# Kernel tuning notes

Hardware: AMD Instinct MI355X
Metric: run time of the kernel (lower is better)

Reference implementation:

```python
import jax, jax.numpy as jnp
import numpy as np

N_NODES = 100000


def _sage_conv(x, src, dst, W_l, b_l, W_r, num_nodes):
    # PyG SAGEConv (aggr='mean'): out = lin_l(mean_j x_j) + lin_r(x)
    msg = x[src]                                                   # [E, d] gather
    s = jax.ops.segment_sum(msg, dst, num_segments=num_nodes)      # [N, d]
    cnt = jax.ops.segment_sum(jnp.ones((src.shape[0], 1), x.dtype), dst,
                              num_segments=num_nodes)              # [N, 1]
    agg = s / jnp.maximum(cnt, 1)                                  # mean, 0 if no neighbors
    return agg @ W_l.T + b_l + x @ W_r.T


def setup_inputs() -> dict:
    key = jax.random.key(0)
    ks = jax.random.split(key, 8)
    d = 64
    E = 1600000
    scale = 1.0 / np.sqrt(d)
    x = jax.random.normal(ks[0], (N_NODES, d), dtype=jnp.float32)
    edge_index = jax.random.randint(ks[1], (2, E), 0, N_NODES, dtype=jnp.int64)
    W1_l = jax.random.normal(ks[2], (d, d), dtype=jnp.float32) * scale
    b1_l = jnp.zeros((d,), dtype=jnp.float32)
    W1_r = jax.random.normal(ks[3], (d, d), dtype=jnp.float32) * scale
    W2_l = jax.random.normal(ks[4], (d, d), dtype=jnp.float32) * scale
    b2_l = jnp.zeros((d,), dtype=jnp.float32)
    W2_r = jax.random.normal(ks[5], (d, d), dtype=jnp.float32) * scale
    return {"x": x, "edge_index": edge_index, "W1_l": W1_l, "b1_l": b1_l,
            "W1_r": W1_r, "W2_l": W2_l, "b2_l": b2_l, "W2_r": W2_r}


def reference(x, edge_index, W1_l, b1_l, W1_r, W2_l, b2_l, W2_r):
    src, dst = edge_index[0], edge_index[1]
    h = jax.nn.relu(_sage_conv(x, src, dst, W1_l, b1_l, W1_r, N_NODES))
    h = jax.nn.relu(_sage_conv(h, src, dst, W2_l, b2_l, W2_r, N_NODES))
    return h
```

## Files before the change

kernel.cpp:

```cpp
#include <hip/hip_runtime.h>
#include <hip/hip_fp16.h>


#define NFEAT 64
#define NPB 128
#define NBUCK 782
#define MAXPB 2560
#define TILE 4096

typedef _Float16 h8 __attribute__((ext_vector_type(8)));
typedef _Float16 h4 __attribute__((ext_vector_type(4)));
typedef float f4 __attribute__((ext_vector_type(4)));
typedef float f2 __attribute__((ext_vector_type(2)));

__device__ inline h8 cvt8f(const float* p) {
  float4 lo = *(const float4*)p;
  float4 hi = *(const float4*)(p + 4);
  h8 f;
  f[0]=(_Float16)lo.x; f[1]=(_Float16)lo.y; f[2]=(_Float16)lo.z; f[3]=(_Float16)lo.w;
  f[4]=(_Float16)hi.x; f[5]=(_Float16)hi.y; f[6]=(_Float16)hi.z; f[7]=(_Float16)hi.w;
  return f;
}

__device__ inline void acc16(float* a, uint4 r) {
  f2 t;
  t = __builtin_amdgcn_cvt_pk_f32_fp8((int)r.x, false); a[0]+=t[0];  a[1]+=t[1];
  t = __builtin_amdgcn_cvt_pk_f32_fp8((int)r.x, true);  a[2]+=t[0];  a[3]+=t[1];
  t = __builtin_amdgcn_cvt_pk_f32_fp8((int)r.y, false); a[4]+=t[0];  a[5]+=t[1];
  t = __builtin_amdgcn_cvt_pk_f32_fp8((int)r.y, true);  a[6]+=t[0];  a[7]+=t[1];
  t = __builtin_amdgcn_cvt_pk_f32_fp8((int)r.z, false); a[8]+=t[0];  a[9]+=t[1];
  t = __builtin_amdgcn_cvt_pk_f32_fp8((int)r.z, true);  a[10]+=t[0]; a[11]+=t[1];
  t = __builtin_amdgcn_cvt_pk_f32_fp8((int)r.w, false); a[12]+=t[0]; a[13]+=t[1];
  t = __builtin_amdgcn_cvt_pk_f32_fp8((int)r.w, true);  a[14]+=t[0]; a[15]+=t[1];
}

__device__ inline void gather_accum(float* a, const int* __restrict__ csr,
                                    const unsigned char* __restrict__ Z,
                                    int start, int deg, int q) {
  int j = 0;
  for (; j + 8 <= deg; j += 8) {
    int idx[8];
#pragma unroll
    for (int k = 0; k < 8; ++k) idx[k] = csr[start + j + k];
    uint4 r[8];
#pragma unroll
    for (int k = 0; k < 8; ++k)
      r[k] = *(const uint4*)(Z + (size_t)idx[k] * NFEAT + q * 16);
#pragma unroll
    for (int k = 0; k < 8; ++k) acc16(a, r[k]);
  }
  for (; j + 4 <= deg; j += 4) {
    int n0 = csr[start + j + 0];
    int n1 = csr[start + j + 1];
    int n2 = csr[start + j + 2];
    int n3 = csr[start + j + 3];
    uint4 r0 = *(const uint4*)(Z + (size_t)n0 * NFEAT + q * 16);
    uint4 r1 = *(const uint4*)(Z + (size_t)n1 * NFEAT + q * 16);
    uint4 r2 = *(const uint4*)(Z + (size_t)n2 * NFEAT + q * 16);
    uint4 r3 = *(const uint4*)(Z + (size_t)n3 * NFEAT + q * 16);
    acc16(a, r0); acc16(a, r1); acc16(a, r2); acc16(a, r3);
  }
  for (; j < deg; ++j) {
    int nb = csr[start + j];
    uint4 r = *(const uint4*)(Z + (size_t)nb * NFEAT + q * 16);
    acc16(a, r);
  }
}

__global__ __launch_bounds__(512) void build_gemm1_k(
    const int* __restrict__ src, const int* __restrict__ dst,
    int* __restrict__ gcur, int* __restrict__ pairs, int E, int sb,
    const float* __restrict__ X, const float* __restrict__ Wl,
    const float* __restrict__ Wr, const float* __restrict__ bias,
    unsigned char* __restrict__ Zf8, __half* __restrict__ Ph, int n) {
  int tid = threadIdx.x;
  if ((int)blockIdx.x < sb) {
    __shared__ int lcnt[NBUCK];
    __shared__ int loff[NBUCK];
    __shared__ int lcur[NBUCK];
    __shared__ int lbase[NBUCK];
    __shared__ int s_packed[TILE];
    __shared__ unsigned short s_b[TILE];

    int tileStart = blockIdx.x * TILE;
    int tileCnt = E - tileStart; if (tileCnt > TILE) tileCnt = TILE;

    for (int t = tid; t < NBUCK; t += 512) lcnt[t] = 0;
    __syncthreads();

    int ep[8], eb[8];
    int base = tileStart + tid * 8;
    int ne = 0;
    if (base + 7 < E) {
      int4 a0 = *(const int4*)(src + base);
      int4 a1 = *(const int4*)(src + base + 4);
      int4 b0 = *(const int4*)(dst + base);
      int4 b1 = *(const int4*)(dst + base + 4);
      int es[8] = {a0.x,a0.y,a0.z,a0.w,a1.x,a1.y,a1.z,a1.w};
      int ed[8] = {b0.x,b0.y,b0.z,b0.w,b1.x,b1.y,b1.z,b1.w};
#pragma unroll
      for (int j = 0; j < 8; ++j) {
        eb[j] = ed[j] >> 7;
        ep[j] = es[j] | ((ed[j] & 127) << 17);
      }
      ne = 8;
    } else {
      for (int j = 0; j < 8 && base + j < E; ++j) {
        int s = src[base + j], d = dst[base + j];
        eb[j] = d >> 7;
        ep[j] = s | ((d & 127) << 17);
        ++ne;
      }
    }
    for (int j = 0; j < ne; ++j) atomicAdd(&lcnt[eb[j]], 1);
    __syncthreads();

    if (tid < 64) {
      int carry = 0;
      for (int cb = 0; cb < NBUCK; cb += 64) {
        int i = cb + tid;
        int v = (i < NBUCK) ? lcnt[i] : 0;
        int x = v;
#pragma unroll
        for (int d = 1; d < 64; d <<= 1) {
          int y = __shfl_up(x, d);
          if (tid >= d) x += y;
        }
        if (i < NBUCK) { int e = x - v + carry; loff[i] = e; lcur[i] = e; }
        carry += __shfl(x, 63);
      }
    }
    __syncthreads();

    for (int t = tid; t < NBUCK; t += 512) {
      int v = lcnt[t];
      if (v) lbase[t] = atomicAdd(&gcur[t], v);
    }
    __syncthreads();

    for (int j = 0; j < ne; ++j) {
      int b = eb[j];
      int slot = atomicAdd(&lcur[b], 1);
      s_packed[slot] = ep[j];
      s_b[slot] = (unsigned short)b;
    }
    __syncthreads();

    for (int k = tid; k < tileCnt; k += 512) {
      int b = s_b[k];
      int g = lbase[b] + (k - loff[b]);
      if (g < MAXPB) pairs[(size_t)b * MAXPB + g] = s_packed[k];
    }
  } else {
    int wave = tid >> 6, lane = tid & 63;
    int m = lane & 15, quad = lane >> 4;
    int row0 = (((int)blockIdx.x - sb) * 8 + wave) * 16;
    if (row0 >= n) return;

    h8 wf[2][4][2];
#pragma unroll
    for (int mat = 0; mat < 2; ++mat) {
      const float* W = mat ? Wr : Wl;
#pragma unroll
      for (int t = 0; t < 4; ++t)
#pragma unroll
        for (int s = 0; s < 2; ++s)
          wf[mat][t][s] = cvt8f(W + (t * 16 + m) * 64 + s * 32 + quad * 8);
    }

    int rowm = row0 + m; if (rowm > n - 1) rowm = n - 1;
    const float* xp = X + (size_t)rowm * 64 + quad * 8;
    h8 af0 = cvt8f(xp);
    h8 af1 = cvt8f(xp + 32);

    f4 accz[4], accp[4];
#pragma unroll
    for (int t = 0; t < 4; ++t) {
      f4 z; z[0]=0.f; z[1]=0.f; z[2]=0.f; z[3]=0.f;
      float4 bl = *(const float4*)(bias + t * 16 + quad * 4);
      f4 p; p[0]=bl.x; p[1]=bl.y; p[2]=bl.z; p[3]=bl.w;
      z = __builtin_amdgcn_mfma_f32_16x16x32_f16(wf[0][t][0], af0, z, 0, 0, 0);
      z = __builtin_amdgcn_mfma_f32_16x16x32_f16(wf[0][t][1], af1, z, 0, 0, 0);
      p = __builtin_amdgcn_mfma_f32_16x16x32_f16(wf[1][t][0], af0, p, 0, 0, 0);
      p = __builtin_amdgcn_mfma_f32_16x16x32_f16(wf[1][t][1], af1, p, 0, 0, 0);
      accz[t] = z;
      accp[t] = p;
    }

    if (row0 + m < n) {
      size_t node = (size_t)(row0 + m);
#pragma unroll
      for (int t = 0; t < 4; ++t) {
        h4 pv;
#pragma unroll
        for (int r = 0; r < 4; ++r) pv[r] = (_Float16)accp[t][r];
        *(h4*)(Ph + node * NFEAT + t * 16 + quad * 4) = pv;
        int v = 0;
        v = __builtin_amdgcn_cvt_pk_fp8_f32(accz[t][0], accz[t][1], v, false);
        v = __builtin_amdgcn_cvt_pk_fp8_f32(accz[t][2], accz[t][3], v, true);
        *(int*)(Zf8 + node * NFEAT + t * 16 + quad * 4) = v;
      }
    }
  }
}

__global__ __launch_bounds__(512) void regroup_k(const int* __restrict__ gcur,
                                                 const int* __restrict__ pairs,
                                                 int* __restrict__ csr,
                                                 int* __restrict__ off,
                                                 int* __restrict__ cnt,
                                                 float* __restrict__ inv, int n) {
  __shared__ int lcnt[NPB];
  __shared__ int lofs[NPB];
  __shared__ int lcur[NPB];
  __shared__ int stage[MAXPB];

  int tid = threadIdx.x;
  int b = blockIdx.x;
  int nbase = b << 7;
  int nn = n - nbase; if (nn > NPB) nn = NPB;
  if (nn <= 0) return;

  int m = gcur[b]; if (m > MAXPB) m = MAXPB;
  const int* seg = pairs + (size_t)b * MAXPB;

  if (tid < NPB) lcnt[tid] = 0;
  __syncthreads();

  for (int e = tid; e < m; e += 512)
    atomicAdd(&lcnt[(seg[e] >> 17) & 127], 1);
  __syncthreads();

  if (tid < 64) {
    int carry = 0;
#pragma unroll
    for (int cb = 0; cb < NPB; cb += 64) {
      int i = cb + tid;
      int v = lcnt[i];
      int x = v;
#pragma unroll
      for (int d = 1; d < 64; d <<= 1) {
        int y = __shfl_up(x, d);
        if (tid >= d) x += y;
      }
      int e = x - v + carry;
      lofs[i] = e; lcur[i] = e;
      carry += __shfl(x, 63);
    }
  }
  __syncthreads();

  for (int e = tid; e < m; e += 512) {
    int p = seg[e];
    int slot = atomicAdd(&lcur[(p >> 17) & 127], 1);
    stage[slot] = p & 0x1FFFF;
  }
  __syncthreads();

  for (int k = tid; k < m; k += 512) csr[(size_t)b * MAXPB + k] = stage[k];
  for (int t = tid; t < nn; t += 512) {
    int c = lcnt[t];
    cnt[nbase + t] = c;
    off[nbase + t] = b * MAXPB + lofs[t];
    inv[nbase + t] = 1.0f / (float)(c > 1 ? c : 1);
  }
}

__global__ __launch_bounds__(256) void aggemm_k(
    const int* __restrict__ off, const int* __restrict__ cnt,
    const float* __restrict__ inv, const int* __restrict__ csr,
    const unsigned char* __restrict__ Z, const __half* __restrict__ Pin,
    const float* __restrict__ Wl, const float* __restrict__ Wr,
    const float* __restrict__ bias,
    unsigned char* __restrict__ Zout, __half* __restrict__ Pout, int n) {
  __shared__ _Float16 Hs[64][72];
  int tid = threadIdx.x;
  int nbase = blockIdx.x * 64;
  int nl = tid >> 2;
  int q  = tid & 3;
  int node = nbase + nl;

  h8 h0, h1;
  if (node < n) {
    float a[16];
#pragma unroll
    for (int i = 0; i < 16; ++i) a[i] = 0.f;
    gather_accum(a, csr, Z, off[node], cnt[node], q);
    float iv = inv[node];
    h8 p0 = *(const h8*)(Pin + (size_t)node * NFEAT + q * 16);
    h8 p1 = *(const h8*)(Pin + (size_t)node * NFEAT + q * 16 + 8);
#pragma unroll
    for (int i = 0; i < 8; ++i)
      h0[i] = (_Float16)fmaxf(fmaf(a[i], iv, (float)p0[i]), 0.f);
#pragma unroll
    for (int i = 0; i < 8; ++i)
      h1[i] = (_Float16)fmaxf(fmaf(a[8 + i], iv, (float)p1[i]), 0.f);
  } else {
#pragma unroll
    for (int i = 0; i < 8; ++i) { h0[i] = (_Float16)0.f; h1[i] = (_Float16)0.f; }
  }
  *(h8*)&Hs[nl][q * 16] = h0;
  *(h8*)&Hs[nl][q * 16 + 8] = h1;

  int wave = tid >> 6, lane = tid & 63;
  int m = lane & 15, quad = lane >> 4;
  int row0 = wave * 16;

  h8 wf[2][4][2];
#pragma unroll
  for (int mat = 0; mat < 2; ++mat) {
    const float* W = mat ? Wr : Wl;
#pragma unroll
    for (int t = 0; t < 4; ++t)
#pragma unroll
      for (int s = 0; s < 2; ++s)
        wf[mat][t][s] = cvt8f(W + (t * 16 + m) * 64 + s * 32 + quad * 8);
  }

  h8 af0 = *(const h8*)&Hs[row0 + m][quad * 8];
  h8 af1 = *(const h8*)&Hs[row0 + m][32 + quad * 8];

  f4 accz[4], accp[4];
#pragma unroll
  for (int t = 0; t < 4; ++t) {
    f4 z; z[0]=0.f; z[1]=0.f; z[2]=0.f; z[3]=0.f;
    float4 bl = *(const float4*)(bias + t * 16 + quad * 4);
    f4 p; p[0]=bl.x; p[1]=bl.y; p[2]=bl.z; p[3]=bl.w;
    z = __builtin_amdgcn_mfma_f32_16x16x32_f16(wf[0][t][0], af0, z, 0, 0, 0);
    z = __builtin_amdgcn_mfma_f32_16x16x32_f16(wf[0][t][1], af1, z, 0, 0, 0);
    p = __builtin_amdgcn_mfma_f32_16x16x32_f16(wf[1][t][0], af0, p, 0, 0, 0);
    p = __builtin_amdgcn_mfma_f32_16x16x32_f16(wf[1][t][1], af1, p, 0, 0, 0);
    accz[t] = z;
    accp[t] = p;
  }

  int gnode = nbase + row0 + m;
  if (gnode < n) {
    size_t nodeix = (size_t)gnode;
#pragma unroll
    for (int t = 0; t < 4; ++t) {
      h4 pv;
#pragma unroll
      for (int r = 0; r < 4; ++r) pv[r] = (_Float16)accp[t][r];
      *(h4*)(Pout + nodeix * NFEAT + t * 16 + quad * 4) = pv;
      int v = 0;
      v = __builtin_amdgcn_cvt_pk_fp8_f32(accz[t][0], accz[t][1], v, false);
      v = __builtin_amdgcn_cvt_pk_fp8_f32(accz[t][2], accz[t][3], v, true);
      *(int*)(Zout + nodeix * NFEAT + t * 16 + quad * 4) = v;
    }
  }
}

__global__ __launch_bounds__(256) void agg2_k(const int* __restrict__ off,
                                              const int* __restrict__ cnt,
                                              const float* __restrict__ inv,
                                              const int* __restrict__ csr,
                                              const unsigned char* __restrict__ Z,
                                              const __half* __restrict__ Pin,
                                              float* __restrict__ out, int n) {
  int t = blockIdx.x * 256 + threadIdx.x;
  int node = t >> 2;
  if (node >= n) return;
  int q = t & 3;

  float a[16];
#pragma unroll
  for (int i = 0; i < 16; ++i) a[i] = 0.f;

  gather_accum(a, csr, Z, off[node], cnt[node], q);

  float iv = inv[node];
  h8 p0 = *(const h8*)(Pin + (size_t)node * NFEAT + q * 16);
  h8 p1 = *(const h8*)(Pin + (size_t)node * NFEAT + q * 16 + 8);

  float4 r0, r1, r2, r3;
  r0.x = fmaxf(fmaf(a[0],  iv, (float)p0[0]), 0.f);
  r0.y = fmaxf(fmaf(a[1],  iv, (float)p0[1]), 0.f);
  r0.z = fmaxf(fmaf(a[2],  iv, (float)p0[2]), 0.f);
  r0.w = fmaxf(fmaf(a[3],  iv, (float)p0[3]), 0.f);
  r1.x = fmaxf(fmaf(a[4],  iv, (float)p0[4]), 0.f);
  r1.y = fmaxf(fmaf(a[5],  iv, (float)p0[5]), 0.f);
  r1.z = fmaxf(fmaf(a[6],  iv, (float)p0[6]), 0.f);
  r1.w = fmaxf(fmaf(a[7],  iv, (float)p0[7]), 0.f);
  r2.x = fmaxf(fmaf(a[8],  iv, (float)p1[0]), 0.f);
  r2.y = fmaxf(fmaf(a[9],  iv, (float)p1[1]), 0.f);
  r2.z = fmaxf(fmaf(a[10], iv, (float)p1[2]), 0.f);
  r2.w = fmaxf(fmaf(a[11], iv, (float)p1[3]), 0.f);
  r3.x = fmaxf(fmaf(a[12], iv, (float)p1[4]), 0.f);
  r3.y = fmaxf(fmaf(a[13], iv, (float)p1[5]), 0.f);
  r3.z = fmaxf(fmaf(a[14], iv, (float)p1[6]), 0.f);
  r3.w = fmaxf(fmaf(a[15], iv, (float)p1[7]), 0.f);

  float* op = out + (size_t)node * NFEAT + q * 16;
  *(float4*)(op + 0)  = r0;
  *(float4*)(op + 4)  = r1;
  *(float4*)(op + 8)  = r2;
  *(float4*)(op + 12) = r3;
}

extern "C" void kernel_launch(void* const* d_in, const int* in_sizes, int n_in,
                              void* d_out, int out_size, void* d_ws, size_t ws_size,
                              hipStream_t stream) {
  const float* x   = (const float*)d_in[0];
  const int*   ei  = (const int*)d_in[1];
  const float* W1l = (const float*)d_in[2];
  const float* b1  = (const float*)d_in[3];
  const float* W1r = (const float*)d_in[4];
  const float* W2l = (const float*)d_in[5];
  const float* b2  = (const float*)d_in[6];
  const float* W2r = (const float*)d_in[7];
  float* out = (float*)d_out;

  int N = in_sizes[0] / NFEAT;
  int E = in_sizes[1] / 2;
  const int* srcp = ei;
  const int* dstp = ei + E;

  char* w = (char*)d_ws;
  int*           pairs = (int*)w;           w += (size_t)NBUCK * MAXPB * 4;
  int*           csr   = (int*)w;           w += (size_t)NBUCK * MAXPB * 4;
  unsigned char* Z1    = (unsigned char*)w; w += (size_t)N * NFEAT;
  __half*        P1    = (__half*)w;        w += (size_t)N * NFEAT * 2;
  unsigned char* Z2    = (unsigned char*)w; w += (size_t)N * NFEAT;
  __half*        P2    = (__half*)w;        w += (size_t)N * NFEAT * 2;
  int*           off   = (int*)w;           w += (size_t)N * 4;
  int*           cnt   = (int*)w;           w += (size_t)N * 4;
  float*         inv   = (float*)w;         w += (size_t)N * 4;
  int*           gcur  = (int*)w;           w += NBUCK * 4;
  if ((size_t)(w - (char*)d_ws) > ws_size) return;

  hipMemsetAsync(gcur, 0, NBUCK * 4, stream);

  int sb  = (E + TILE - 1) / TILE;
  int gb1 = (N + 127) / 128;

  build_gemm1_k<<<sb + gb1, 512, 0, stream>>>(srcp, dstp, gcur, pairs, E, sb,
                                              x, W1l, W1r, b1, Z1, P1, N);
  regroup_k<<<NBUCK, 512, 0, stream>>>(gcur, pairs, csr, off, cnt, inv, N);
  aggemm_k<<<(N + 63) / 64, 256, 0, stream>>>(off, cnt, inv, csr, Z1, P1,
                                              W2l, W2r, b2, Z2, P2, N);
  agg2_k<<<(N * 4 + 255) / 256, 256, 0, stream>>>(off, cnt, inv, csr, Z2, P2,
                                                  out, N);
}
```

Measured before the change: 232.3 us.

## Split layer-2 features into halves, team-parallel gather, nontemporal loads/stores

Stores the layer-2 FP8 feature table as two 32-byte planes so the final aggregation kernel runs one plane per block pass. Each plane's rows are smaller and more cache-friendly. Each node is handled by 8 threads, with 4 teams splitting the edge list and reducing via shuffles. Many streaming loads and stores are made nontemporal, the 8-way unrolled gather loop is removed, and a __syncthreads is added before the shared-memory GEMM read. The split adds a second pass over the CSR indices and extra shuffle work.

```diff
diff --git a/kernel.cpp b/kernel.cpp
--- a/kernel.cpp
+++ b/kernel.cpp
@@ -12,6 +12,30 @@
 typedef _Float16 h4 __attribute__((ext_vector_type(4)));
 typedef float f4 __attribute__((ext_vector_type(4)));
 typedef float f2 __attribute__((ext_vector_type(2)));
+typedef int i4 __attribute__((ext_vector_type(4)));
+typedef unsigned int u4 __attribute__((ext_vector_type(4)));
+typedef unsigned int u2 __attribute__((ext_vector_type(2)));
+
+__device__ inline int ntload_i(const int* p) { return __builtin_nontemporal_load(p); }
+__device__ inline float ntload_f(const float* p) { return __builtin_nontemporal_load(p); }
+__device__ inline i4 ntload_i4(const int* p) {
+  return __builtin_nontemporal_load((const i4*)p);
+}
+__device__ inline f4 ntload_f4(const float* p) {
+  return __builtin_nontemporal_load((const f4*)p);
+}
+__device__ inline h8 ntload_h8(const __half* p) {
+  u4 v = __builtin_nontemporal_load((const u4*)p);
+  return *(h8*)&v;
+}
+__device__ inline void ntstore_i(int* p, int v) { __builtin_nontemporal_store(v, p); }
+__device__ inline void ntstore_f4(float* p, f4 v) {
+  __builtin_nontemporal_store(v, (f4*)p);
+}
+__device__ inline void ntstore_h4(__half* p, h4 v) {
+  u2 u = *(u2*)&v;
+  __builtin_nontemporal_store(u, (u2*)p);
+}
 
 __device__ inline h8 cvt8f(const float* p) {
   float4 lo = *(const float4*)p;
@@ -19,6 +43,15 @@
   h8 f;
   f[0]=(_Float16)lo.x; f[1]=(_Float16)lo.y; f[2]=(_Float16)lo.z; f[3]=(_Float16)lo.w;
   f[4]=(_Float16)hi.x; f[5]=(_Float16)hi.y; f[6]=(_Float16)hi.z; f[7]=(_Float16)hi.w;
+  return f;
+}
+
+__device__ inline h8 cvt8f_nt(const float* p) {
+  f4 lo = ntload_f4(p);
+  f4 hi = ntload_f4(p + 4);
+  h8 f;
+  f[0]=(_Float16)lo[0]; f[1]=(_Float16)lo[1]; f[2]=(_Float16)lo[2]; f[3]=(_Float16)lo[3];
+  f[4]=(_Float16)hi[0]; f[5]=(_Float16)hi[1]; f[6]=(_Float16)hi[2]; f[7]=(_Float16)hi[3];
   return f;
 }
 
@@ -38,22 +71,11 @@
                                     const unsigned char* __restrict__ Z,
                                     int start, int deg, int q) {
   int j = 0;
-  for (; j + 8 <= deg; j += 8) {
-    int idx[8];
-#pragma unroll
-    for (int k = 0; k < 8; ++k) idx[k] = csr[start + j + k];
-    uint4 r[8];
-#pragma unroll
-    for (int k = 0; k < 8; ++k)
-      r[k] = *(const uint4*)(Z + (size_t)idx[k] * NFEAT + q * 16);
-#pragma unroll
-    for (int k = 0; k < 8; ++k) acc16(a, r[k]);
-  }
   for (; j + 4 <= deg; j += 4) {
-    int n0 = csr[start + j + 0];
-    int n1 = csr[start + j + 1];
-    int n2 = csr[start + j + 2];
-    int n3 = csr[start + j + 3];
+    int n0 = ntload_i(csr + start + j + 0);
+    int n1 = ntload_i(csr + start + j + 1);
+    int n2 = ntload_i(csr + start + j + 2);
+    int n3 = ntload_i(csr + start + j + 3);
     uint4 r0 = *(const uint4*)(Z + (size_t)n0 * NFEAT + q * 16);
     uint4 r1 = *(const uint4*)(Z + (size_t)n1 * NFEAT + q * 16);
     uint4 r2 = *(const uint4*)(Z + (size_t)n2 * NFEAT + q * 16);
@@ -61,7 +83,7 @@
     acc16(a, r0); acc16(a, r1); acc16(a, r2); acc16(a, r3);
   }
   for (; j < deg; ++j) {
-    int nb = csr[start + j];
+    int nb = ntload_i(csr + start + j);
     uint4 r = *(const uint4*)(Z + (size_t)nb * NFEAT + q * 16);
     acc16(a, r);
   }
@@ -92,12 +114,12 @@
     int base = tileStart + tid * 8;
     int ne = 0;
     if (base + 7 < E) {
-      int4 a0 = *(const int4*)(src + base);
-      int4 a1 = *(const int4*)(src + base + 4);
-      int4 b0 = *(const int4*)(dst + base);
-      int4 b1 = *(const int4*)(dst + base + 4);
-      int es[8] = {a0.x,a0.y,a0.z,a0.w,a1.x,a1.y,a1.z,a1.w};
-      int ed[8] = {b0.x,b0.y,b0.z,b0.w,b1.x,b1.y,b1.z,b1.w};
+      i4 a0 = ntload_i4(src + base);
+      i4 a1 = ntload_i4(src + base + 4);
+      i4 b0 = ntload_i4(dst + base);
+      i4 b1 = ntload_i4(dst + base + 4);
+      int es[8] = {a0[0],a0[1],a0[2],a0[3],a1[0],a1[1],a1[2],a1[3]};
+      int ed[8] = {b0[0],b0[1],b0[2],b0[3],b1[0],b1[1],b1[2],b1[3]};
 #pragma unroll
       for (int j = 0; j < 8; ++j) {
         eb[j] = ed[j] >> 7;
@@ -149,7 +171,7 @@
     for (int k = tid; k < tileCnt; k += 512) {
       int b = s_b[k];
       int g = lbase[b] + (k - loff[b]);
-      if (g < MAXPB) pairs[(size_t)b * MAXPB + g] = s_packed[k];
+      if (g < MAXPB) ntstore_i(&pairs[(size_t)b * MAXPB + g], s_packed[k]);
     }
   } else {
     int wave = tid >> 6, lane = tid & 63;
@@ -170,8 +192,8 @@
 
     int rowm = row0 + m; if (rowm > n - 1) rowm = n - 1;
     const float* xp = X + (size_t)rowm * 64 + quad * 8;
-    h8 af0 = cvt8f(xp);
-    h8 af1 = cvt8f(xp + 32);
+    h8 af0 = cvt8f_nt(xp);
+    h8 af1 = cvt8f_nt(xp + 32);
 
     f4 accz[4], accp[4];
 #pragma unroll
@@ -257,7 +279,7 @@
   }
   __syncthreads();
 
-  for (int k = tid; k < m; k += 512) csr[(size_t)b * MAXPB + k] = stage[k];
+  for (int k = tid; k < m; k += 512) ntstore_i(&csr[(size_t)b * MAXPB + k], stage[k]);
   for (int t = tid; t < nn; t += 512) {
     int c = lcnt[t];
     cnt[nbase + t] = c;
@@ -272,7 +294,8 @@
     const unsigned char* __restrict__ Z, const __half* __restrict__ Pin,
     const float* __restrict__ Wl, const float* __restrict__ Wr,
     const float* __restrict__ bias,
-    unsigned char* __restrict__ Zout, __half* __restrict__ Pout, int n) {
+    unsigned char* __restrict__ Zlo, unsigned char* __restrict__ Zhi,
+    __half* __restrict__ Pout, int n) {
   __shared__ _Float16 Hs[64][72];
   int tid = threadIdx.x;
   int nbase = blockIdx.x * 64;
@@ -285,10 +308,10 @@
     float a[16];
 #pragma unroll
     for (int i = 0; i < 16; ++i) a[i] = 0.f;
-    gather_accum(a, csr, Z, off[node], cnt[node], q);
-    float iv = inv[node];
-    h8 p0 = *(const h8*)(Pin + (size_t)node * NFEAT + q * 16);
-    h8 p1 = *(const h8*)(Pin + (size_t)node * NFEAT + q * 16 + 8);
+    gather_accum(a, csr, Z, ntload_i(off + node), ntload_i(cnt + node), q);
+    float iv = ntload_f(inv + node);
+    h8 p0 = ntload_h8(Pin + (size_t)node * NFEAT + q * 16);
+    h8 p1 = ntload_h8(Pin + (size_t)node * NFEAT + q * 16 + 8);
 #pragma unroll
     for (int i = 0; i < 8; ++i)
       h0[i] = (_Float16)fmaxf(fmaf(a[i], iv, (float)p0[i]), 0.f);
@@ -301,6 +324,7 @@
   }
   *(h8*)&Hs[nl][q * 16] = h0;
   *(h8*)&Hs[nl][q * 16 + 8] = h1;
+  __syncthreads();
 
   int wave = tid >> 6, lane = tid & 63;
   int m = lane & 15, quad = lane >> 4;
@@ -342,11 +366,12 @@
       h4 pv;
 #pragma unroll
       for (int r = 0; r < 4; ++r) pv[r] = (_Float16)accp[t][r];
-      *(h4*)(Pout + nodeix * NFEAT + t * 16 + quad * 4) = pv;
+      ntstore_h4(Pout + nodeix * NFEAT + t * 16 + quad * 4, pv);
       int v = 0;
       v = __builtin_amdgcn_cvt_pk_fp8_f32(accz[t][0], accz[t][1], v, false);
       v = __builtin_amdgcn_cvt_pk_fp8_f32(accz[t][2], accz[t][3], v, true);
-      *(int*)(Zout + nodeix * NFEAT + t * 16 + quad * 4) = v;
+      unsigned char* zp = (t < 2) ? Zlo : Zhi;
+      ntstore_i((int*)(zp + nodeix * 32 + (t & 1) * 16 + quad * 4), v);
     }
   }
 }
@@ -355,47 +380,84 @@
                                               const int* __restrict__ cnt,
                                               const float* __restrict__ inv,
                                               const int* __restrict__ csr,
-                                              const unsigned char* __restrict__ Z,
+                                              const unsigned char* __restrict__ Zlo,
+                                              const unsigned char* __restrict__ Zhi,
                                               const __half* __restrict__ Pin,
-                                              float* __restrict__ out, int n) {
-  int t = blockIdx.x * 256 + threadIdx.x;
-  int node = t >> 2;
+                                              float* __restrict__ out,
+                                              int n, int nchunk) {
+  int bi = blockIdx.x;
+  int plane = (bi >= nchunk) ? 1 : 0;
+  int chunk = plane ? bi - nchunk : bi;
+  int tid = threadIdx.x;
+  int nl = tid >> 3;
+  int node = chunk * 32 + nl;
   if (node >= n) return;
-  int q = t & 3;
+  int t8   = tid & 7;
+  int half = t8 & 1;
+  int team = t8 >> 1;
+  const unsigned char* Zp = plane ? Zhi : Zlo;
 
   float a[16];
 #pragma unroll
   for (int i = 0; i < 16; ++i) a[i] = 0.f;
 
-  gather_accum(a, csr, Z, off[node], cnt[node], q);
-
-  float iv = inv[node];
-  h8 p0 = *(const h8*)(Pin + (size_t)node * NFEAT + q * 16);
-  h8 p1 = *(const h8*)(Pin + (size_t)node * NFEAT + q * 16 + 8);
-
-  float4 r0, r1, r2, r3;
-  r0.x = fmaxf(fmaf(a[0],  iv, (float)p0[0]), 0.f);
-  r0.y = fmaxf(fmaf(a[1],  iv, (float)p0[1]), 0.f);
-  r0.z = fmaxf(fmaf(a[2],  iv, (float)p0[2]), 0.f);
-  r0.w = fmaxf(fmaf(a[3],  iv, (float)p0[3]), 0.f);
-  r1.x = fmaxf(fmaf(a[4],  iv, (float)p0[4]), 0.f);
-  r1.y = fmaxf(fmaf(a[5],  iv, (float)p0[5]), 0.f);
-  r1.z = fmaxf(fmaf(a[6],  iv, (float)p0[6]), 0.f);
-  r1.w = fmaxf(fmaf(a[7],  iv, (float)p0[7]), 0.f);
-  r2.x = fmaxf(fmaf(a[8],  iv, (float)p1[0]), 0.f);
-  r2.y = fmaxf(fmaf(a[9],  iv, (float)p1[1]), 0.f);
-  r2.z = fmaxf(fmaf(a[10], iv, (float)p1[2]), 0.f);
-  r2.w = fmaxf(fmaf(a[11], iv, (float)p1[3]), 0.f);
-  r3.x = fmaxf(fmaf(a[12], iv, (float)p1[4]), 0.f);
-  r3.y = fmaxf(fmaf(a[13], iv, (float)p1[5]), 0.f);
-  r3.z = fmaxf(fmaf(a[14], iv, (float)p1[6]), 0.f);
-  r3.w = fmaxf(fmaf(a[15], iv, (float)p1[7]), 0.f);
-
-  float* op = out + (size_t)node * NFEAT + q * 16;
-  *(float4*)(op + 0)  = r0;
-  *(float4*)(op + 4)  = r1;
-  *(float4*)(op + 8)  = r2;
-  *(float4*)(op + 12) = r3;
+  int start = ntload_i(off + node);
+  int deg = ntload_i(cnt + node);
+  int nfull = deg >> 2;
+  for (int k = team; k < nfull; k += 4) {
+    int j = start + k * 4;
+    int n0 = ntload_i(csr + j + 0);
+    int n1 = ntload_i(csr + j + 1);
+    int n2 = ntload_i(csr + j + 2);
+    int n3 = ntload_i(csr + j + 3);
+    uint4 r0 = *(const uint4*)(Zp + (size_t)n0 * 32 + half * 16);
+    uint4 r1 = *(const uint4*)(Zp + (size_t)n1 * 32 + half * 16);
+    uint4 r2 = *(const uint4*)(Zp + (size_t)n2 * 32 + half * 16);
+    uint4 r3 = *(const uint4*)(Zp + (size_t)n3 * 32 + half * 16);
+    acc16(a, r0); acc16(a, r1); acc16(a, r2); acc16(a, r3);
+  }
+  int rem = deg & 3;
+  if (rem && ((nfull & 3) == team)) {
+    int j = start + nfull * 4;
+    for (int i = 0; i < rem; ++i) {
+      int nb = ntload_i(csr + j + i);
+      uint4 r = *(const uint4*)(Zp + (size_t)nb * 32 + half * 16);
+      acc16(a, r);
+    }
+  }
+#pragma unroll
+  for (int i = 0; i < 16; ++i) a[i] += __shfl_xor(a[i], 2);
+#pragma unroll
+  for (int i = 0; i < 16; ++i) a[i] += __shfl_xor(a[i], 4);
+
+  if (team == 0) {
+    float iv = ntload_f(inv + node);
+    int fbase = plane * 32 + half * 16;
+    h8 p0 = ntload_h8(Pin + (size_t)node * NFEAT + fbase);
+    h8 p1 = ntload_h8(Pin + (size_t)node * NFEAT + fbase + 8);
+    f4 r0, r1, r2, r3;
+    r0[0] = fmaxf(fmaf(a[0],  iv, (float)p0[0]), 0.f);
+    r0[1] = fmaxf(fmaf(a[1],  iv, (float)p0[1]), 0.f);
+    r0[2] = fmaxf(fmaf(a[2],  iv, (float)p0[2]), 0.f);
+    r0[3] = fmaxf(fmaf(a[3],  iv, (float)p0[3]), 0.f);
+    r1[0] = fmaxf(fmaf(a[4],  iv, (float)p0[4]), 0.f);
+    r1[1] = fmaxf(fmaf(a[5],  iv, (float)p0[5]), 0.f);
+    r1[2] = fmaxf(fmaf(a[6],  iv, (float)p0[6]), 0.f);
+    r1[3] = fmaxf(fmaf(a[7],  iv, (float)p0[7]), 0.f);
+    r2[0] = fmaxf(fmaf(a[8],  iv, (float)p1[0]), 0.f);
+    r2[1] = fmaxf(fmaf(a[9],  iv, (float)p1[1]), 0.f);
+    r2[2] = fmaxf(fmaf(a[10], iv, (float)p1[2]), 0.f);
+    r2[3] = fmaxf(fmaf(a[11], iv, (float)p1[3]), 0.f);
+    r3[0] = fmaxf(fmaf(a[12], iv, (float)p1[4]), 0.f);
+    r3[1] = fmaxf(fmaf(a[13], iv, (float)p1[5]), 0.f);
+    r3[2] = fmaxf(fmaf(a[14], iv, (float)p1[6]), 0.f);
+    r3[3] = fmaxf(fmaf(a[15], iv, (float)p1[7]), 0.f);
+    float* op = out + (size_t)node * NFEAT + fbase;
+    ntstore_f4(op + 0,  r0);
+    ntstore_f4(op + 4,  r1);
+    ntstore_f4(op + 8,  r2);
+    ntstore_f4(op + 12, r3);
+  }
 }
 
 extern "C" void kernel_launch(void* const* d_in, const int* in_sizes, int n_in,
@@ -429,16 +491,20 @@
   int*           gcur  = (int*)w;           w += NBUCK * 4;
   if ((size_t)(w - (char*)d_ws) > ws_size) return;
 
+  unsigned char* Z2lo = Z2;
+  unsigned char* Z2hi = Z2 + (size_t)N * 32;
+
   hipMemsetAsync(gcur, 0, NBUCK * 4, stream);
 
   int sb  = (E + TILE - 1) / TILE;
   int gb1 = (N + 127) / 128;
+  int nchunk = (N + 31) / 32;
 
   build_gemm1_k<<<sb + gb1, 512, 0, stream>>>(srcp, dstp, gcur, pairs, E, sb,
                                               x, W1l, W1r, b1, Z1, P1, N);
   regroup_k<<<NBUCK, 512, 0, stream>>>(gcur, pairs, csr, off, cnt, inv, N);
   aggemm_k<<<(N + 63) / 64, 256, 0, stream>>>(off, cnt, inv, csr, Z1, P1,
-                                              W2l, W2r, b2, Z2, P2, N);
-  agg2_k<<<(N * 4 + 255) / 256, 256, 0, stream>>>(off, cnt, inv, csr, Z2, P2,
-                                                  out, N);
-}
+                                              W2l, W2r, b2, Z2lo, Z2hi, P2, N);
+  agg2_k<<<2 * nchunk, 256, 0, stream>>>(off, cnt, inv, csr, Z2lo, Z2hi, P2,
+                                         out, N, nchunk);
+}
```

After: 259.1 us. 1.12x slower.
